# Kernel optimization log

Measured on AMD Instinct MI355X. Metric: run time of the kernel, lower is better.

The kernel has to match this reference:

```python
import jax, jax.numpy as jnp
import numpy as np

DIM = 768
HEADS = 8
HEAD_DIM = DIM // HEADS
SCALE = DIM ** (-0.5)  # faithful: original scales by dimension**-0.5, not head_dim


def setup_inputs() -> dict:
    key = jax.random.key(0)
    k1, k2, k3 = jax.random.split(key, 3)
    B, N = 2, 4096
    x = jax.random.normal(k1, (B, N, DIM), dtype=jnp.float32)
    # qkv projection params (Linear(dim, 3*dim))
    W_qkv = jax.random.normal(k2, (DIM, 3 * DIM), dtype=jnp.float32) * (DIM ** -0.5)
    b_qkv = jax.random.normal(k3, (3 * DIM,), dtype=jnp.float32) * 0.01
    return {"x": x, "W_qkv": W_qkv, "b_qkv": b_qkv}


def reference(x, W_qkv, b_qkv):
    B, N, D = x.shape
    qkv = x @ W_qkv + b_qkv                       # (B, N, 3D)
    qkv = qkv.reshape(B, N, 3, HEADS, HEAD_DIM)
    q, k, v = jnp.moveaxis(qkv, 2, 0)             # each (B, N, H, dh)
    # (B, H, N, N) scores — explicit materialization as in the source
    scores = jnp.einsum('bnhd,bmhd->bhnm', q, k) * SCALE
    attn = jax.nn.softmax(scores, axis=-1)
    out = jnp.einsum('bhnm,bmhd->bnhd', attn, v)  # (B, N, H, dh)
    return out.reshape(B, N, D)
```

## Files before the change

### kernel.cpp

```cpp
#include <hip/hip_runtime.h>
#include <hip/hip_bf16.h>


typedef __attribute__((ext_vector_type(8)))  short    bf16x8;
typedef __attribute__((ext_vector_type(4)))  float    floatx4;
typedef __attribute__((ext_vector_type(16))) float    floatx16;
typedef __attribute__((ext_vector_type(8)))  unsigned short us8;
typedef __attribute__((ext_vector_type(4)))  unsigned short us4;

#define HEADS 8
#define DH 96
#define NSEQ 4096
#define DIM 768
#define SCALE2_F (0.03608439182435161f * 1.4426950408889634f)

#define GLOAD16(g, s) __builtin_amdgcn_global_load_lds(                              \
    (const __attribute__((address_space(1))) unsigned int*)(g),                      \
    (__attribute__((address_space(3))) unsigned int*)(s), 16, 0, 0)

__device__ __forceinline__ unsigned short f2bf(float f) {
    union { float f; unsigned u; } v; v.f = f;
    unsigned r = v.u + 0x7fffu + ((v.u >> 16) & 1u);
    return (unsigned short)(r >> 16);
}

__device__ __forceinline__ unsigned pk2(float a, float b) {
    float2 t; t.x = a; t.y = b;
    __hip_bfloat162 r = __float22bfloat162_rn(t);
    return *(unsigned*)&r;
}

__device__ __forceinline__ bf16x8 mk_pfrag(float c0, float c1, float c2, float c3,
                                           float c4, float c5, float c6, float c7, int hB) {
    unsigned pl0 = pk2(c0, c1), pl1 = pk2(c2, c3);
    unsigned pu0 = pk2(c4, c5), pu1 = pk2(c6, c7);
    unsigned s0 = hB ? pl0 : pu0, s1 = hB ? pl1 : pu1;
    unsigned r0 = (unsigned)__shfl_xor((int)s0, 32);
    unsigned r1 = (unsigned)__shfl_xor((int)s1, 32);
    union { unsigned u[4]; bf16x8 v; } f;
    f.u[0] = hB ? r0 : pl0;
    f.u[1] = hB ? r1 : pl1;
    f.u[2] = hB ? pu0 : r0;
    f.u[3] = hB ? pu1 : r1;
    return f.v;
}

__global__ __launch_bounds__(256) void cvt(const float* __restrict__ x,
                                           const float* __restrict__ w,
                                           unsigned short* __restrict__ xb,
                                           unsigned short* __restrict__ wt) {
    __shared__ unsigned short sm[64][33];
    const int bid = blockIdx.x;
    const int t = threadIdx.x;
    if (bid < 6144) {
        int i = bid * 256 + t;
        float4 v = ((const float4*)x)[i];
        us4 o; o.x = f2bf(v.x); o.y = f2bf(v.y); o.z = f2bf(v.z); o.w = f2bf(v.w);
        ((us4*)xb)[i] = o;
    } else {
        int wb = bid - 6144;
        int c0 = (wb % 72) * 32, k0 = (wb / 72) * 64;
        int cl = t & 31, kl0 = t >> 5;
        for (int i = 0; i < 8; ++i) {
            int kl = kl0 + i * 8;
            sm[kl][cl] = f2bf(w[(k0 + kl) * 2304 + c0 + cl]);
        }
        __syncthreads();
        int kl2 = t & 63, cl0 = t >> 6;
        for (int i = 0; i < 8; ++i) {
            int cl2 = cl0 + i * 4;
            wt[(c0 + cl2) * 768 + k0 + kl2] = sm[kl2][cl2];
        }
    }
}

__global__ __launch_bounds__(256) void gemm_qkv(const unsigned short* __restrict__ xb,
                                                const unsigned short* __restrict__ wt,
                                                const float* __restrict__ bias,
                                                unsigned short* __restrict__ qb,
                                                unsigned short* __restrict__ kb,
                                                unsigned short* __restrict__ vt) {
    __shared__ unsigned short As[2][128 * 64];
    __shared__ unsigned short Bs[2][128 * 64];
    const int tid = threadIdx.x;
    const int lane = tid & 63, wv = tid >> 6;
    const int n15 = lane & 15, quad = lane >> 4;
    const int x7q = n15 & 7;
    const int mw = (wv >> 1) * 64, nw = (wv & 1) * 64;
    const int lrow = lane >> 3;
    const int lcolsw = ((lane & 7) ^ lrow) * 8;
    const int lofs = wv * 8 * 64;
    floatx4 acc[4][4] = {};

    const int raw = blockIdx.x;
    const int id = (raw & 7) * 144 + (raw >> 3);
    const bool isv = id >= 768;
    int m0, c0;
    const unsigned short *gA, *gB;
    if (!isv) {
        m0 = (id / 12) * 128; c0 = (id % 12) * 128;
        gA = xb + (size_t)(m0 + wv * 8 + lrow) * 768 + lcolsw;
        gB = wt + (size_t)(c0 + wv * 8 + lrow) * 768 + lcolsw;
    } else {
        int iv = id - 768;
        c0 = (iv / 6) * 128; m0 = (iv % 6) * 128;
        gA = wt + (size_t)(1536 + m0 + wv * 8 + lrow) * 768 + lcolsw;
        gB = xb + (size_t)(c0 + wv * 8 + lrow) * 768 + lcolsw;
    }

    auto stage = [&](int b, int kt) {
#pragma unroll
        for (int i = 0; i < 4; ++i) {
            GLOAD16(gA + (size_t)i * 32 * 768 + kt * 64, &As[b][lofs + i * 32 * 64]);
            GLOAD16(gB + (size_t)i * 32 * 768 + kt * 64, &Bs[b][lofs + i * 32 * 64]);
        }
    };

    stage(0, 0);
    __syncthreads();
#pragma unroll 2
    for (int kt = 0; kt < 12; ++kt) {
        const int cur = kt & 1;
        if (kt < 11) stage(cur ^ 1, kt + 1);
#pragma unroll
        for (int ks = 0; ks < 2; ++ks) {
            bf16x8 af[4], bfr[4];
            for (int mt = 0; mt < 4; ++mt)
                af[mt] = *(const bf16x8*)&As[cur][(mw + mt * 16 + n15) * 64
                                                 + (((ks << 2) + quad) ^ x7q) * 8];
            for (int nt = 0; nt < 4; ++nt)
                bfr[nt] = *(const bf16x8*)&Bs[cur][(nw + nt * 16 + n15) * 64
                                                  + (((ks << 2) + quad) ^ x7q) * 8];
            for (int mt = 0; mt < 4; ++mt)
                for (int nt = 0; nt < 4; ++nt)
                    acc[mt][nt] = __builtin_amdgcn_mfma_f32_16x16x32_bf16(af[mt], bfr[nt], acc[mt][nt], 0, 0, 0);
        }
        __syncthreads();
    }

    if (!isv) {
        for (int nt = 0; nt < 4; ++nt) {
            int c = c0 + nw + nt * 16 + n15;
            float bv = bias[c];
            int which = c / 768, rem = c % 768;
            int h = rem / 96, d = rem % 96;
            for (int mt = 0; mt < 4; ++mt) {
                for (int r = 0; r < 4; ++r) {
                    int m = m0 + mw + mt * 16 + quad * 4 + r;
                    int b = m >> 12, n = m & 4095;
                    float val = acc[mt][nt][r] + bv;
                    int bh = b * HEADS + h;
                    if (which == 0) qb[(bh * NSEQ + n) * DH + d] = f2bf(val * SCALE2_F);
                    else            kb[(bh * NSEQ + n) * DH + d] = f2bf(val);
                }
            }
        }
    } else {
        for (int mt = 0; mt < 4; ++mt) {
            for (int r = 0; r < 4; ++r) {
                int dv = m0 + mw + mt * 16 + quad * 4 + r;
                float bv = bias[1536 + dv];
                int h = dv / 96, d = dv % 96;
                for (int nt = 0; nt < 4; ++nt) {
                    int ng = c0 + nw + nt * 16 + n15;
                    int b = ng >> 12, n = ng & 4095;
                    vt[((size_t)(b * HEADS + h) * DH + d) * NSEQ + n] = f2bf(acc[mt][nt][r] + bv);
                }
            }
        }
    }
}

template<int SPLIT>
__global__ __launch_bounds__(256, 2) void flash(const unsigned short* __restrict__ qb,
                                                const unsigned short* __restrict__ kb,
                                                const unsigned short* __restrict__ vt,
                                                float* __restrict__ outp,
                                                float* __restrict__ lp) {
    __shared__ unsigned short sm[34816];
    __shared__ float l_all[128];

    const int tid = threadIdx.x;
    const int lane = tid & 63, wv = tid >> 6;
    const int l31 = lane & 31, h = lane >> 5;
    const int x7 = l31 & 7;
    const int idg = blockIdx.x;
    const int half = SPLIT ? (idg >> 9) : 0;
    const int id = SPLIT ? (idg & 511) : idg;
    const int bh = id & 15;
    const int q0 = (id >> 4) * 128 + wv * 32;
    const int NT = SPLIT ? 32 : 64;

    const unsigned short* kgb = kb + (size_t)bh * NSEQ * DH + (size_t)half * 2048 * DH;
    const unsigned short* vgb = vt + (size_t)bh * DH * NSEQ + (size_t)half * 2048;

    bf16x8 qf[6];
    {
        const unsigned short* qrow = qb + (size_t)(bh * NSEQ + q0 + l31) * DH;
#pragma unroll
        for (int ks = 0; ks < 6; ++ks)
            qf[ks] = *(const bf16x8*)&qrow[ks * 16 + h * 8];
    }

    int kofs[2][6];
#pragma unroll
    for (int kt = 0; kt < 2; ++kt)
#pragma unroll
        for (int ks = 0; ks < 6; ++ks) {
            int b = 2 * ks + h;
            int bs = (b < 8) ? (b ^ x7) : (8 + ((b - 8) ^ x7));
            kofs[kt][ks] = (kt * 32 + l31) * 128 + bs * 8;
        }
    int vofs[3][4];
#pragma unroll
    for (int dt = 0; dt < 3; ++dt)
#pragma unroll
        for (int s = 0; s < 4; ++s)
            vofs[dt][s] = (dt * 32 + l31) * 64 + ((2 * s + h) ^ x7) * 8;

    int goffk[3], goffv[3], wofk[3], wofv[3];
#pragma unroll
    for (int i = 0; i < 3; ++i) {
        int tb = i * 256 + tid;
        int r = tb / 12, bb = tb % 12;
        goffk[i] = r * 96 + bb * 8;
        int bs = (bb < 8) ? (bb ^ (r & 7)) : (8 + ((bb - 8) ^ (r & 7)));
        wofk[i] = r * 128 + bs * 8;
        int d = tb >> 3, b2 = tb & 7;
        goffv[i] = d * 4096 + b2 * 8;
        wofv[i] = d * 64 + ((b2 ^ (d & 7))) * 8;
    }

    const floatx16 z16 = (floatx16)(0.f);

    us8 kr[3], vr[3];
    const unsigned short* kpf = kgb;
    const unsigned short* vpf = vgb;
#pragma unroll
    for (int i = 0; i < 3; ++i) { kr[i] = *(const us8*)&kpf[goffk[i]]; vr[i] = *(const us8*)&vpf[goffv[i]]; }
    kpf += 6144; vpf += 64;
#pragma unroll
    for (int i = 0; i < 3; ++i) { *(us8*)&sm[wofk[i]] = kr[i]; *(us8*)&sm[16384 + wofv[i]] = vr[i]; }
#pragma unroll
    for (int i = 0; i < 3; ++i) { kr[i] = *(const us8*)&kpf[goffk[i]]; vr[i] = *(const us8*)&vpf[goffv[i]]; }
    kpf += 6144; vpf += 64;
    __syncthreads();

    floatx16 stA[2], stB[2];
#pragma unroll
    for (int ks = 0; ks < 6; ++ks)
#pragma unroll
        for (int kt = 0; kt < 2; ++kt) {
            bf16x8 ak = *(const bf16x8*)&sm[kofs[kt][ks]];
            stA[kt] = __builtin_amdgcn_mfma_f32_32x32x16_bf16(ak, qf[ks], ks == 0 ? z16 : stA[kt], 0, 0, 0);
        }

    floatx16 o[3] = {};
    float lsum = 0.f;

    auto body = [&](int kv, floatx16 (&cur)[2], floatx16 (&nxt)[2]) {
        if (kv < NT - 1) {
            unsigned short* Kd = sm + ((kv + 1) & 1) * 8192;
            unsigned short* Vd = sm + 16384 + ((kv + 1) % 3) * 6144;
#pragma unroll
            for (int i = 0; i < 3; ++i) { *(us8*)&Kd[wofk[i]] = kr[i]; *(us8*)&Vd[wofv[i]] = vr[i]; }
            if (kv < NT - 2) {
#pragma unroll
                for (int i = 0; i < 3; ++i) { kr[i] = *(const us8*)&kpf[goffk[i]]; vr[i] = *(const us8*)&vpf[goffv[i]]; }
                kpf += 6144; vpf += 64;
            }
        }
        __syncthreads();

        if (kv < NT - 1) {
            const unsigned short* Kn = sm + ((kv + 1) & 1) * 8192;
#pragma unroll
            for (int ks = 0; ks < 6; ++ks)
#pragma unroll
                for (int kt = 0; kt < 2; ++kt) {
                    bf16x8 ak = *(const bf16x8*)&Kn[kofs[kt][ks]];
                    nxt[kt] = __builtin_amdgcn_mfma_f32_32x32x16_bf16(ak, qf[ks], ks == 0 ? z16 : nxt[kt], 0, 0, 0);
                }
        }

#pragma unroll
        for (int kt = 0; kt < 2; ++kt)
#pragma unroll
            for (int rg = 0; rg < 16; ++rg) {
                float p = __builtin_amdgcn_exp2f(cur[kt][rg]);
                cur[kt][rg] = p;
                lsum += p;
            }
        bf16x8 pf[4];
        pf[0] = mk_pfrag(cur[0][0], cur[0][1], cur[0][2], cur[0][3],
                         cur[0][4], cur[0][5], cur[0][6], cur[0][7], h);
        pf[1] = mk_pfrag(cur[0][8], cur[0][9], cur[0][10], cur[0][11],
                         cur[0][12], cur[0][13], cur[0][14], cur[0][15], h);
        pf[2] = mk_pfrag(cur[1][0], cur[1][1], cur[1][2], cur[1][3],
                         cur[1][4], cur[1][5], cur[1][6], cur[1][7], h);
        pf[3] = mk_pfrag(cur[1][8], cur[1][9], cur[1][10], cur[1][11],
                         cur[1][12], cur[1][13], cur[1][14], cur[1][15], h);

        const unsigned short* Vc = sm + 16384 + (kv % 3) * 6144;
#pragma unroll
        for (int s = 0; s < 4; ++s)
#pragma unroll
            for (int dt = 0; dt < 3; ++dt) {
                bf16x8 bv = *(const bf16x8*)&Vc[vofs[dt][s]];
                o[dt] = __builtin_amdgcn_mfma_f32_32x32x16_bf16(pf[s], bv, o[dt], 0, 0, 0);
            }
    };

    for (int kv = 0; kv < NT; kv += 2) {
        body(kv, stA, stB);
        body(kv + 1, stB, stA);
    }

    lsum += __shfl_xor(lsum, 32);
    const int b = bh >> 3, hd = bh & 7;

    if (SPLIT) {
        if (h == 0) lp[(size_t)(half * 16 + bh) * NSEQ + q0 + l31] = lsum;
        float* ob = outp + (size_t)half * (2 * NSEQ * DIM);
#pragma unroll
        for (int rg = 0; rg < 16; ++rg) {
            int row = (rg & 3) + 8 * (rg >> 2) + 4 * h;
            int q = q0 + row;
            float* op = ob + (size_t)(b * NSEQ + q) * DIM + hd * DH;
#pragma unroll
            for (int dt = 0; dt < 3; ++dt)
                op[dt * 32 + l31] = o[dt][rg];
        }
    } else {
        if (h == 0) l_all[wv * 32 + l31] = lsum;
        __syncthreads();
#pragma unroll
        for (int rg = 0; rg < 16; ++rg) {
            int row = (rg & 3) + 8 * (rg >> 2) + 4 * h;
            float inv = 1.0f / l_all[wv * 32 + row];
            int q = q0 + row;
            float* op = outp + (size_t)(b * NSEQ + q) * DIM + hd * DH;
#pragma unroll
            for (int dt = 0; dt < 3; ++dt)
                op[dt * 32 + l31] = o[dt][rg] * inv;
        }
    }
}

__global__ __launch_bounds__(256) void combine(const float* __restrict__ P,
                                               const float* __restrict__ ls,
                                               float* __restrict__ out) {
    int i = blockIdx.x * 256 + threadIdx.x;
    int row = i / 192;
    int hd = (i % 192) / 24;
    int b = row >> 12, q = row & 4095;
    int bh = b * HEADS + hd;
    float l = ls[bh * NSEQ + q] + ls[16 * NSEQ + bh * NSEQ + q];
    float inv = 1.0f / l;
    float4 v0 = ((const float4*)P)[i];
    float4 v1 = ((const float4*)P)[1572864 + i];
    float4 r;
    r.x = (v0.x + v1.x) * inv;
    r.y = (v0.y + v1.y) * inv;
    r.z = (v0.z + v1.z) * inv;
    r.w = (v0.w + v1.w) * inv;
    ((float4*)out)[i] = r;
}

extern "C" void kernel_launch(void* const* d_in, const int* in_sizes, int n_in,
                              void* d_out, int out_size, void* d_ws, size_t ws_size,
                              hipStream_t stream) {
    const float* x    = (const float*)d_in[0];
    const float* W    = (const float*)d_in[1];
    const float* bias = (const float*)d_in[2];
    float* out = (float*)d_out;

    char* ws = (char*)d_ws;
    unsigned short* xb = (unsigned short*)(ws);
    unsigned short* wt = (unsigned short*)(ws + 12582912);
    unsigned short* qb = (unsigned short*)(ws + 16121856);
    unsigned short* kb = (unsigned short*)(ws + 28704768);
    unsigned short* vt = (unsigned short*)(ws + 41287680);
    float* Opart = (float*)(ws + 53870592);
    float* lpart = (float*)(ws + 104202240);
    const size_t WS_NEED = 104726528;

    cvt<<<7008, 256, 0, stream>>>(x, W, xb, wt);
    gemm_qkv<<<1152, 256, 0, stream>>>(xb, wt, bias, qb, kb, vt);
    if (ws_size >= WS_NEED) {
        flash<1><<<1024, 256, 0, stream>>>(qb, kb, vt, Opart, lpart);
        combine<<<6144, 256, 0, stream>>>(Opart, lpart, out);
    } else {
        flash<0><<<512, 256, 0, stream>>>(qb, kb, vt, out, nullptr);
    }
}
```

Baseline: 263.9 us.

## Use 8-wave 512-thread flash blocks sharing each K/V tile across 256 queries

Adds a flash8 kernel for the split-KV path that launches 512-thread blocks of 8 waves, covering 256 query rows per block instead of 128. Each K/V tile staged in LDS is therefore reused by twice as many query rows, and the global load of each tile is spread across 512 threads with each thread loading a mix of K and V pieces. The aim is to halve K/V global traffic and LDS staging work per query. In exchange each barrier now synchronises 8 waves, and the launch bound of 4 blocks of 512 threads tightens the per-thread register budget. The non-split fallback is de-templated but otherwise unchanged.

```diff
diff --git a/kernel.cpp b/kernel.cpp
--- a/kernel.cpp
+++ b/kernel.cpp
@@ -171,28 +171,190 @@
     }
 }
 
-template<int SPLIT>
-__global__ __launch_bounds__(256, 2) void flash(const unsigned short* __restrict__ qb,
-                                                const unsigned short* __restrict__ kb,
-                                                const unsigned short* __restrict__ vt,
-                                                float* __restrict__ outp,
-                                                float* __restrict__ lp) {
+__global__ __launch_bounds__(512, 4) void flash8(const unsigned short* __restrict__ qb,
+                                                 const unsigned short* __restrict__ kb,
+                                                 const unsigned short* __restrict__ vt,
+                                                 float* __restrict__ outp,
+                                                 float* __restrict__ lp) {
     __shared__ unsigned short sm[34816];
-    __shared__ float l_all[128];
 
     const int tid = threadIdx.x;
     const int lane = tid & 63, wv = tid >> 6;
     const int l31 = lane & 31, h = lane >> 5;
     const int x7 = l31 & 7;
-    const int idg = blockIdx.x;
-    const int half = SPLIT ? (idg >> 9) : 0;
-    const int id = SPLIT ? (idg & 511) : idg;
+    const int id = blockIdx.x;
+    const int bh = id & 15;
+    const int half = (id >> 4) & 1;
+    const int q0 = (id >> 5) * 256 + wv * 32;
+    const int NT = 32;
+
+    const unsigned short* kgb = kb + (size_t)bh * NSEQ * DH + (size_t)half * 2048 * DH;
+    const unsigned short* vgb = vt + (size_t)bh * DH * NSEQ + (size_t)half * 2048;
+
+    bf16x8 qf[6];
+    {
+        const unsigned short* qrow = qb + (size_t)(bh * NSEQ + q0 + l31) * DH;
+#pragma unroll
+        for (int ks = 0; ks < 6; ++ks)
+            qf[ks] = *(const bf16x8*)&qrow[ks * 16 + h * 8];
+    }
+
+    int kofs[2][6];
+#pragma unroll
+    for (int kt = 0; kt < 2; ++kt)
+#pragma unroll
+        for (int ks = 0; ks < 6; ++ks) {
+            int b = 2 * ks + h;
+            int bs = (b < 8) ? (b ^ x7) : (8 + ((b - 8) ^ x7));
+            kofs[kt][ks] = (kt * 32 + l31) * 128 + bs * 8;
+        }
+    int vofs[3][4];
+#pragma unroll
+    for (int dt = 0; dt < 3; ++dt)
+#pragma unroll
+        for (int s = 0; s < 4; ++s)
+            vofs[dt][s] = (dt * 32 + l31) * 64 + ((2 * s + h) ^ x7) * 8;
+
+    const unsigned short* gptr[3];
+    int step[3], wofs[3], wbase[3];
+#pragma unroll
+    for (int i = 0; i < 3; ++i) {
+        int tb = i * 512 + tid;
+        if (tb < 768) {
+            int r = tb / 12, bb = tb % 12;
+            gptr[i] = kgb + r * 96 + bb * 8;
+            step[i] = 6144;
+            int bs = (bb < 8) ? (bb ^ (r & 7)) : (8 + ((bb - 8) ^ (r & 7)));
+            wofs[i] = r * 128 + bs * 8;
+            wbase[i] = 0;
+        } else {
+            int c = tb - 768;
+            int d = c / 8, b2 = c & 7;
+            gptr[i] = vgb + d * 4096 + b2 * 8;
+            step[i] = 64;
+            wofs[i] = d * 64 + ((b2 ^ (d & 7))) * 8;
+            wbase[i] = 1;
+        }
+    }
+
+    const floatx16 z16 = (floatx16)(0.f);
+
+    us8 st[3];
+#pragma unroll
+    for (int i = 0; i < 3; ++i) { st[i] = *(const us8*)gptr[i]; gptr[i] += step[i]; }
+#pragma unroll
+    for (int i = 0; i < 3; ++i) {
+        unsigned short* dst = sm + (wbase[i] ? 16384 : 0) + wofs[i];
+        *(us8*)dst = st[i];
+    }
+#pragma unroll
+    for (int i = 0; i < 3; ++i) { st[i] = *(const us8*)gptr[i]; gptr[i] += step[i]; }
+    __syncthreads();
+
+    floatx16 stA[2], stB[2];
+#pragma unroll
+    for (int ks = 0; ks < 6; ++ks)
+#pragma unroll
+        for (int kt = 0; kt < 2; ++kt) {
+            bf16x8 ak = *(const bf16x8*)&sm[kofs[kt][ks]];
+            stA[kt] = __builtin_amdgcn_mfma_f32_32x32x16_bf16(ak, qf[ks], ks == 0 ? z16 : stA[kt], 0, 0, 0);
+        }
+
+    floatx16 o[3] = {};
+    float lsum = 0.f;
+
+    auto body = [&](int kv, floatx16 (&cur)[2], floatx16 (&nxt)[2]) {
+        if (kv < NT - 1) {
+            const int kslot = ((kv + 1) & 1) * 8192;
+            const int vslot = 16384 + ((kv + 1) % 3) * 6144;
+#pragma unroll
+            for (int i = 0; i < 3; ++i) {
+                unsigned short* dst = sm + (wbase[i] ? vslot : kslot) + wofs[i];
+                *(us8*)dst = st[i];
+            }
+            if (kv < NT - 2) {
+#pragma unroll
+                for (int i = 0; i < 3; ++i) { st[i] = *(const us8*)gptr[i]; gptr[i] += step[i]; }
+            }
+        }
+        __syncthreads();
+
+        if (kv < NT - 1) {
+            const unsigned short* Kn = sm + ((kv + 1) & 1) * 8192;
+#pragma unroll
+            for (int ks = 0; ks < 6; ++ks)
+#pragma unroll
+                for (int kt = 0; kt < 2; ++kt) {
+                    bf16x8 ak = *(const bf16x8*)&Kn[kofs[kt][ks]];
+                    nxt[kt] = __builtin_amdgcn_mfma_f32_32x32x16_bf16(ak, qf[ks], ks == 0 ? z16 : nxt[kt], 0, 0, 0);
+                }
+        }
+
+#pragma unroll
+        for (int kt = 0; kt < 2; ++kt)
+#pragma unroll
+            for (int rg = 0; rg < 16; ++rg) {
+                float p = __builtin_amdgcn_exp2f(cur[kt][rg]);
+                cur[kt][rg] = p;
+                lsum += p;
+            }
+        bf16x8 pf[4];
+        pf[0] = mk_pfrag(cur[0][0], cur[0][1], cur[0][2], cur[0][3],
+                         cur[0][4], cur[0][5], cur[0][6], cur[0][7], h);
+        pf[1] = mk_pfrag(cur[0][8], cur[0][9], cur[0][10], cur[0][11],
+                         cur[0][12], cur[0][13], cur[0][14], cur[0][15], h);
+        pf[2] = mk_pfrag(cur[1][0], cur[1][1], cur[1][2], cur[1][3],
+                         cur[1][4], cur[1][5], cur[1][6], cur[1][7], h);
+        pf[3] = mk_pfrag(cur[1][8], cur[1][9], cur[1][10], cur[1][11],
+                         cur[1][12], cur[1][13], cur[1][14], cur[1][15], h);
+
+        const unsigned short* Vc = sm + 16384 + (kv % 3) * 6144;
+#pragma unroll
+        for (int s = 0; s < 4; ++s)
+#pragma unroll
+            for (int dt = 0; dt < 3; ++dt) {
+                bf16x8 bv = *(const bf16x8*)&Vc[vofs[dt][s]];
+                o[dt] = __builtin_amdgcn_mfma_f32_32x32x16_bf16(pf[s], bv, o[dt], 0, 0, 0);
+            }
+    };
+
+    for (int kv = 0; kv < NT; kv += 2) {
+        body(kv, stA, stB);
+        body(kv + 1, stB, stA);
+    }
+
+    lsum += __shfl_xor(lsum, 32);
+    const int b = bh >> 3, hd = bh & 7;
+    if (h == 0) lp[(size_t)(half * 16 + bh) * NSEQ + q0 + l31] = lsum;
+    float* ob = outp + (size_t)half * (2 * NSEQ * DIM);
+#pragma unroll
+    for (int rg = 0; rg < 16; ++rg) {
+        int row = (rg & 3) + 8 * (rg >> 2) + 4 * h;
+        int q = q0 + row;
+        float* op = ob + (size_t)(b * NSEQ + q) * DIM + hd * DH;
+#pragma unroll
+        for (int dt = 0; dt < 3; ++dt)
+            op[dt * 32 + l31] = o[dt][rg];
+    }
+}
+
+__global__ __launch_bounds__(256, 2) void flash(const unsigned short* __restrict__ qb,
+                                                const unsigned short* __restrict__ kb,
+                                                const unsigned short* __restrict__ vt,
+                                                float* __restrict__ outp) {
+    __shared__ unsigned short sm[34816];
+    __shared__ float l_all[128];
+
+    const int tid = threadIdx.x;
+    const int lane = tid & 63, wv = tid >> 6;
+    const int l31 = lane & 31, h = lane >> 5;
+    const int x7 = l31 & 7;
+    const int id = blockIdx.x;
     const int bh = id & 15;
     const int q0 = (id >> 4) * 128 + wv * 32;
-    const int NT = SPLIT ? 32 : 64;
-
-    const unsigned short* kgb = kb + (size_t)bh * NSEQ * DH + (size_t)half * 2048 * DH;
-    const unsigned short* vgb = vt + (size_t)bh * DH * NSEQ + (size_t)half * 2048;
+
+    const unsigned short* kgb = kb + (size_t)bh * NSEQ * DH;
+    const unsigned short* vgb = vt + (size_t)bh * DH * NSEQ;
 
     bf16x8 qf[6];
     {
@@ -259,12 +421,12 @@
     float lsum = 0.f;
 
     auto body = [&](int kv, floatx16 (&cur)[2], floatx16 (&nxt)[2]) {
-        if (kv < NT - 1) {
+        if (kv < 63) {
             unsigned short* Kd = sm + ((kv + 1) & 1) * 8192;
             unsigned short* Vd = sm + 16384 + ((kv + 1) % 3) * 6144;
 #pragma unroll
             for (int i = 0; i < 3; ++i) { *(us8*)&Kd[wofk[i]] = kr[i]; *(us8*)&Vd[wofv[i]] = vr[i]; }
-            if (kv < NT - 2) {
+            if (kv < 62) {
 #pragma unroll
                 for (int i = 0; i < 3; ++i) { kr[i] = *(const us8*)&kpf[goffk[i]]; vr[i] = *(const us8*)&vpf[goffv[i]]; }
                 kpf += 6144; vpf += 64;
@@ -272,7 +434,7 @@
         }
         __syncthreads();
 
-        if (kv < NT - 1) {
+        if (kv < 63) {
             const unsigned short* Kn = sm + ((kv + 1) & 1) * 8192;
 #pragma unroll
             for (int ks = 0; ks < 6; ++ks)
@@ -311,39 +473,25 @@
             }
     };
 
-    for (int kv = 0; kv < NT; kv += 2) {
+    for (int kv = 0; kv < 64; kv += 2) {
         body(kv, stA, stB);
         body(kv + 1, stB, stA);
     }
 
     lsum += __shfl_xor(lsum, 32);
+    if (h == 0) l_all[wv * 32 + l31] = lsum;
+    __syncthreads();
+
     const int b = bh >> 3, hd = bh & 7;
-
-    if (SPLIT) {
-        if (h == 0) lp[(size_t)(half * 16 + bh) * NSEQ + q0 + l31] = lsum;
-        float* ob = outp + (size_t)half * (2 * NSEQ * DIM);
-#pragma unroll
-        for (int rg = 0; rg < 16; ++rg) {
-            int row = (rg & 3) + 8 * (rg >> 2) + 4 * h;
-            int q = q0 + row;
-            float* op = ob + (size_t)(b * NSEQ + q) * DIM + hd * DH;
-#pragma unroll
-            for (int dt = 0; dt < 3; ++dt)
-                op[dt * 32 + l31] = o[dt][rg];
-        }
-    } else {
-        if (h == 0) l_all[wv * 32 + l31] = lsum;
-        __syncthreads();
-#pragma unroll
-        for (int rg = 0; rg < 16; ++rg) {
-            int row = (rg & 3) + 8 * (rg >> 2) + 4 * h;
-            float inv = 1.0f / l_all[wv * 32 + row];
-            int q = q0 + row;
-            float* op = outp + (size_t)(b * NSEQ + q) * DIM + hd * DH;
-#pragma unroll
-            for (int dt = 0; dt < 3; ++dt)
-                op[dt * 32 + l31] = o[dt][rg] * inv;
-        }
+#pragma unroll
+    for (int rg = 0; rg < 16; ++rg) {
+        int row = (rg & 3) + 8 * (rg >> 2) + 4 * h;
+        float inv = 1.0f / l_all[wv * 32 + row];
+        int q = q0 + row;
+        float* op = outp + (size_t)(b * NSEQ + q) * DIM + hd * DH;
+#pragma unroll
+        for (int dt = 0; dt < 3; ++dt)
+            op[dt * 32 + l31] = o[dt][rg] * inv;
     }
 }
 
@@ -388,9 +536,9 @@
     cvt<<<7008, 256, 0, stream>>>(x, W, xb, wt);
     gemm_qkv<<<1152, 256, 0, stream>>>(xb, wt, bias, qb, kb, vt);
     if (ws_size >= WS_NEED) {
-        flash<1><<<1024, 256, 0, stream>>>(qb, kb, vt, Opart, lpart);
+        flash8<<<512, 512, 0, stream>>>(qb, kb, vt, Opart, lpart);
         combine<<<6144, 256, 0, stream>>>(Opart, lpart, out);
     } else {
-        flash<0><<<512, 256, 0, stream>>>(qb, kb, vt, out, nullptr);
-    }
-}
+        flash<<<512, 256, 0, stream>>>(qb, kb, vt, out);
+    }
+}
```

Result: slower. 732.3 us (+177.4%).
